# Optimization experiments

Hardware: AMD Instinct MI355X
Metric: run time of the kernel (lower is better)

The kernel has to match this reference:

```python
import jax, jax.numpy as jnp
import numpy as np

C, N, KS = 64, 64, 3  # channels, spatial size, kernel size (matches init_kwargs)
B = 4


def identity_kernel(c, k):
    # 'full' identity kernel: delta at spatial center on the channel diagonal
    ker = np.zeros((c, c, k, k), np.float32)
    ker[np.arange(c), np.arange(c), k // 2, k // 2] = 1.0
    return jnp.asarray(ker)


def setup_inputs() -> dict:
    key = jax.random.key(0)
    k1, k2, k3 = jax.random.split(key, 3)
    conv_in = jax.random.normal(k1, (B, C, N, N), jnp.float32)
    # small kernel perturbation, as produced by a hypernetwork at near-init ('I + net')
    K = jax.random.normal(k2, (B, C, C, KS, KS), jnp.float32) * 0.05
    bias = jax.random.normal(k3, (B, C, 1, 1), jnp.float32)
    return {"conv_in": conv_in, "K": K, "bias": bias}


def _circ_conv_one(x, ker):
    # x: [c, n, n], ker: [co, ci, kh, kw]; circular-padded cross-correlation (torch conv2d semantics)
    p = KS // 2
    xp = jnp.pad(x, ((0, 0), (p, p), (p, p)), mode="wrap")
    out = jax.lax.conv_general_dilated(
        xp[None], ker, window_strides=(1, 1), padding="VALID",
        dimension_numbers=("NCHW", "OIHW", "NCHW"))
    return out[0]  # [c, n, n]


def reference(conv_in, K, bias):
    # kernel_init == 'I + net': add identity kernel
    Kfull = K + identity_kernel(C, KS)[None]  # [B, c, c, k, k]

    # batch spatial circular conv2D with per-sample kernels
    conv_out = jax.vmap(_circ_conv_one)(conv_in, Kfull) + bias  # [B, c, n, n]

    # spectral log-determinant of the circular conv operator:
    # embed kernel into n x n grid, FFT2 over space, then per-frequency c x c logdet.
    # (per-frequency phase factors from kernel centering have unit modulus, so
    #  log|det| is independent of the spatial alignment convention)
    Kpad = jnp.zeros((K.shape[0], C, C, N, N), K.dtype).at[..., :KS, :KS].set(Kfull)
    Khat = jnp.fft.fft2(Kpad)                    # [B, c, c, n, n] complex
    Khat = jnp.moveaxis(Khat, (1, 2), (3, 4))    # [B, n, n, c, c]
    _, logabsdet = jnp.linalg.slogdet(Khat)      # [B, n, n]
    logdet = jnp.sum(logabsdet, axis=(1, 2))     # [B]

    return conv_out, logdet
```

## Files before the change

### kernel.cpp

```cpp
#include <hip/hip_runtime.h>
#include <hip/hip_fp16.h>
#include <math.h>

#define CCH 64
#define NSP 64
#define TAU 0.5f

__global__ __launch_bounds__(256) void conv_kernel(
    const float* __restrict__ x, const float* __restrict__ K,
    const float* __restrict__ bias, float* __restrict__ out) {
  int bid = blockIdx.x;
  int b = bid >> 6, co = bid & 63;
  __shared__ float w[CCH * 9];
  __shared__ float tile[64 * 65];
  int t = threadIdx.x;

  for (int i = t; i < CCH * 9; i += 256) {
    float v = K[(size_t)((b * 64 + co) * 64) * 9 + i];
    if (i == co * 9 + 4) v += 1.0f;
    w[i] = v;
  }

  int ty = t >> 2;
  int tx = t & 3;
  int x0 = tx << 4;
  float bval = bias[b * 64 + co];
  float acc[16];
#pragma unroll
  for (int i = 0; i < 16; ++i) acc[i] = bval;

  const float* xb = x + (size_t)(b * 64) * 4096;
  for (int ci = 0; ci < 64; ++ci) {
    __syncthreads();
    const float* xc = xb + (size_t)ci * 4096;
#pragma unroll
    for (int j = 0; j < 16; ++j) {
      int i = t + 256 * j;
      tile[(i >> 6) * 65 + (i & 63)] = xc[i];
    }
    __syncthreads();

    float w0 = w[ci * 9 + 0], w1 = w[ci * 9 + 1], w2 = w[ci * 9 + 2];
    float w3 = w[ci * 9 + 3], w4 = w[ci * 9 + 4], w5 = w[ci * 9 + 5];
    float w6 = w[ci * 9 + 6], w7 = w[ci * 9 + 7], w8 = w[ci * 9 + 8];

    int ym = ((ty - 1) & 63) * 65;
    int yc = ty * 65;
    int yp = ((ty + 1) & 63) * 65;
    float in0[18], in1[18], in2[18];
#pragma unroll
    for (int ix = 0; ix < 18; ++ix) {
      int xx = (x0 + ix - 1) & 63;
      in0[ix] = tile[ym + xx];
      in1[ix] = tile[yc + xx];
      in2[ix] = tile[yp + xx];
    }
#pragma unroll
    for (int px = 0; px < 16; ++px) {
      float a = acc[px];
      a = fmaf(w0, in0[px], a); a = fmaf(w1, in0[px + 1], a); a = fmaf(w2, in0[px + 2], a);
      a = fmaf(w3, in1[px], a); a = fmaf(w4, in1[px + 1], a); a = fmaf(w5, in1[px + 2], a);
      a = fmaf(w6, in2[px], a); a = fmaf(w7, in2[px + 1], a); a = fmaf(w8, in2[px + 2], a);
      acc[px] = a;
    }
  }

  float* op = out + (size_t)(b * 64 + co) * 4096 + ty * 64 + x0;
#pragma unroll
  for (int i = 0; i < 16; i += 4) {
    *(float4*)(op + i) = make_float4(acc[i], acc[i + 1], acc[i + 2], acc[i + 3]);
  }
}

__device__ __forceinline__ int h2i(__half2 h) { int i; __builtin_memcpy(&i, &h, 4); return i; }
__device__ __forceinline__ __half2 i2h(int i) { __half2 h; __builtin_memcpy(&h, &i, 4); return h; }

__global__ __launch_bounds__(64, 3) void logdet_kernel(
    const float* __restrict__ K, float* __restrict__ logdet) {
  int bid = blockIdx.x;
  int u, v;
  if (bid < 33) { u = 0; v = bid; }
  else if (bid < 2017) { int q = bid - 33; u = 1 + (q >> 6); v = q & 63; }
  else { u = 32; v = bid - 2017; }
  float weight = (((u & 31) == 0) && ((v & 31) == 0)) ? 1.0f : 2.0f;
  int b = blockIdx.y;

  int r = threadIdx.x;

  float Ar[3], Ai[3], Br[3], Bi[3];
  {
    const float k2pi = -6.283185307179586f / 64.0f;
    float su, cu, sv, cv;
    __sincosf(k2pi * (float)u, &su, &cu);
    __sincosf(k2pi * (float)v, &sv, &cv);
    Ar[0] = 1.0f; Ai[0] = 0.0f; Ar[1] = cu; Ai[1] = su;
    Ar[2] = cu * cu - su * su; Ai[2] = 2.0f * cu * su;
    Br[0] = 1.0f; Bi[0] = 0.0f; Br[1] = cv; Bi[1] = sv;
    Br[2] = cv * cv - sv * sv; Bi[2] = 2.0f * cv * sv;
  }
  float wr[9], wi[9];
#pragma unroll
  for (int kh = 0; kh < 3; ++kh)
#pragma unroll
    for (int kw = 0; kw < 3; ++kw) {
      wr[kh * 3 + kw] = Ar[kh] * Br[kw] - Ai[kh] * Bi[kw];
      wi[kh * 3 + kw] = Ar[kh] * Bi[kw] + Ai[kh] * Br[kw];
    }

  __half2 a2[65];
  const float4* Kp4 = (const float4*)(K + (size_t)(b * 64 + r) * 576);
#pragma unroll
  for (int g = 0; g < 16; ++g) {
    float f[36];
#pragma unroll
    for (int qq = 0; qq < 9; ++qq) {
      float4 vv = Kp4[g * 9 + qq];
      f[qq * 4 + 0] = vv.x; f[qq * 4 + 1] = vv.y; f[qq * 4 + 2] = vv.z; f[qq * 4 + 3] = vv.w;
    }
#pragma unroll
    for (int cc = 0; cc < 4; ++cc) {
      int c = g * 4 + cc;
      float re = 0.0f, im = 0.0f;
#pragma unroll
      for (int t9 = 0; t9 < 9; ++t9) {
        float kv = f[cc * 9 + t9];
        re = fmaf(kv, wr[t9], re);
        im = fmaf(kv, wi[t9], im);
      }
      if (c == r) { re += wr[4]; im += wi[4]; }
      a2[c] = __floats2half2_rn(re, im);
    }
  }
  a2[64] = __floats2half2_rn(0.0f, 0.0f);

  bool active = true;
  float pivmag = 1.0f;

  for (int k = 0; k < 63; ++k) {
    float fr0 = __low2float(a2[0]);
    float fi0 = __high2float(a2[0]);
    float mag = fmaf(fr0, fr0, fi0 * fi0);
    bool cand = active && (mag >= TAU);
    unsigned long long candm = __ballot(cand);
    int p;
    if (candm != 0ULL) {
      p = __ffsll(candm) - 1;
    } else {
      float mm = active ? mag : -1.0f;
#pragma unroll
      for (int off = 32; off > 0; off >>= 1) mm = fmaxf(mm, __shfl_xor(mm, off));
      unsigned long long mx = __ballot(active && (mag == mm));
      if (mx == 0ULL) mx = __ballot(active);
      p = __ffsll(mx) - 1;
    }
    p = __builtin_amdgcn_readfirstlane(p) & 63;

    bool isPiv = (r == p);
    pivmag = isPiv ? mag : pivmag;
    active = active && !isPiv;

    __half2 pivh = i2h(__builtin_amdgcn_readlane(h2i(a2[0]), p));
    float pr = __low2float(pivh);
    float pi = __high2float(pivh);
    float inv = __builtin_amdgcn_rcpf(fmaf(pr, pr, pi * pi));
    float fre = (fr0 * pr + fi0 * pi) * inv;
    float fim = (fi0 * pr - fr0 * pi) * inv;
    fre = active ? fre : 0.0f;
    fim = active ? fim : 0.0f;
    __half2 nfre2 = __float2half2_rn(-fre);
    __half2 fim2 = __halves2half2(__float2half_rn(fim),
                                  __float2half_rn(-fim));

    int rem = 63 - k;
#pragma unroll
    for (int ch = 0; ch < 8; ++ch) {
      if (ch * 8 < rem) {
        int c0 = ch * 8 + 1;
        int Li[8];
#pragma unroll
        for (int e = 0; e < 8; ++e)
          Li[e] = __builtin_amdgcn_readlane(h2i(a2[c0 + e]), p);
#pragma unroll
        for (int e = 0; e < 8; ++e) {
          __half2 P = i2h(Li[e]);
          __half2 tmp = __hfma2(nfre2, P, a2[c0 + e]);
          a2[c0 + e - 1] = __hfma2(fim2, __lowhigh2highlow(P), tmp);
        }
      }
    }
  }
  {
    float fr0 = __low2float(a2[0]);
    float fi0 = __high2float(a2[0]);
    if (active) pivmag = fmaf(fr0, fr0, fi0 * fi0);
  }

  float logsum = 0.5f * __logf(pivmag);
#pragma unroll
  for (int off = 32; off > 0; off >>= 1) logsum += __shfl_xor(logsum, off);
  if (r == 0) atomicAdd(&logdet[b], weight * logsum);
}

extern "C" void kernel_launch(void* const* d_in, const int* in_sizes, int n_in,
                              void* d_out, int out_size, void* d_ws, size_t ws_size,
                              hipStream_t stream) {
  const float* conv_in = (const float*)d_in[0];
  const float* K       = (const float*)d_in[1];
  const float* bias    = (const float*)d_in[2];
  float* out = (float*)d_out;
  float* logdet = out + 1048576;

  hipMemsetAsync(logdet, 0, 4 * sizeof(float), stream);
  conv_kernel<<<dim3(256), dim3(256), 0, stream>>>(conv_in, K, bias, out);
  logdet_kernel<<<dim3(2050, 4), dim3(64), 0, stream>>>(K, logdet);
}
```

Before: 371.7 us.

## Fuse conv and logdet into one launch with interleaved block roles

Merges the convolution kernel and the spectral logdet kernel into a single launch. Every ninth block performs a conv output channel and the rest perform logdet frequencies, so the two workloads run on the GPU at the same time. Each logdet block now handles all four batch samples for one frequency, one wavefront per sample, instead of one 64-thread block per (frequency, batch) pair. This removes a launch and the serialization between the two kernels. In exchange, the register budget is now shared between both roles under launch bounds of (256, 2), which could reduce occupancy or cause spills in the register-heavy logdet path.

```diff
diff --git a/kernel.cpp b/kernel.cpp
--- a/kernel.cpp
+++ b/kernel.cpp
@@ -2,90 +2,100 @@
 #include <hip/hip_fp16.h>
 #include <math.h>
 
-#define CCH 64
-#define NSP 64
 #define TAU 0.5f
-
-__global__ __launch_bounds__(256) void conv_kernel(
-    const float* __restrict__ x, const float* __restrict__ K,
-    const float* __restrict__ bias, float* __restrict__ out) {
-  int bid = blockIdx.x;
-  int b = bid >> 6, co = bid & 63;
-  __shared__ float w[CCH * 9];
-  __shared__ float tile[64 * 65];
-  int t = threadIdx.x;
-
-  for (int i = t; i < CCH * 9; i += 256) {
-    float v = K[(size_t)((b * 64 + co) * 64) * 9 + i];
-    if (i == co * 9 + 4) v += 1.0f;
-    w[i] = v;
-  }
-
-  int ty = t >> 2;
-  int tx = t & 3;
-  int x0 = tx << 4;
-  float bval = bias[b * 64 + co];
-  float acc[16];
-#pragma unroll
-  for (int i = 0; i < 16; ++i) acc[i] = bval;
-
-  const float* xb = x + (size_t)(b * 64) * 4096;
-  for (int ci = 0; ci < 64; ++ci) {
-    __syncthreads();
-    const float* xc = xb + (size_t)ci * 4096;
-#pragma unroll
-    for (int j = 0; j < 16; ++j) {
-      int i = t + 256 * j;
-      tile[(i >> 6) * 65 + (i & 63)] = xc[i];
-    }
-    __syncthreads();
-
-    float w0 = w[ci * 9 + 0], w1 = w[ci * 9 + 1], w2 = w[ci * 9 + 2];
-    float w3 = w[ci * 9 + 3], w4 = w[ci * 9 + 4], w5 = w[ci * 9 + 5];
-    float w6 = w[ci * 9 + 6], w7 = w[ci * 9 + 7], w8 = w[ci * 9 + 8];
-
-    int ym = ((ty - 1) & 63) * 65;
-    int yc = ty * 65;
-    int yp = ((ty + 1) & 63) * 65;
-    float in0[18], in1[18], in2[18];
-#pragma unroll
-    for (int ix = 0; ix < 18; ++ix) {
-      int xx = (x0 + ix - 1) & 63;
-      in0[ix] = tile[ym + xx];
-      in1[ix] = tile[yc + xx];
-      in2[ix] = tile[yp + xx];
-    }
-#pragma unroll
-    for (int px = 0; px < 16; ++px) {
-      float a = acc[px];
-      a = fmaf(w0, in0[px], a); a = fmaf(w1, in0[px + 1], a); a = fmaf(w2, in0[px + 2], a);
-      a = fmaf(w3, in1[px], a); a = fmaf(w4, in1[px + 1], a); a = fmaf(w5, in1[px + 2], a);
-      a = fmaf(w6, in2[px], a); a = fmaf(w7, in2[px + 1], a); a = fmaf(w8, in2[px + 2], a);
-      acc[px] = a;
-    }
-  }
-
-  float* op = out + (size_t)(b * 64 + co) * 4096 + ty * 64 + x0;
-#pragma unroll
-  for (int i = 0; i < 16; i += 4) {
-    *(float4*)(op + i) = make_float4(acc[i], acc[i + 1], acc[i + 2], acc[i + 3]);
-  }
-}
 
 __device__ __forceinline__ int h2i(__half2 h) { int i; __builtin_memcpy(&i, &h, 4); return i; }
 __device__ __forceinline__ __half2 i2h(int i) { __half2 h; __builtin_memcpy(&h, &i, 4); return h; }
 
-__global__ __launch_bounds__(64, 3) void logdet_kernel(
-    const float* __restrict__ K, float* __restrict__ logdet) {
+__global__ __launch_bounds__(256, 2) void fused_kernel(
+    const float* __restrict__ x, const float* __restrict__ K,
+    const float* __restrict__ bias, float* __restrict__ out,
+    float* __restrict__ logdet) {
+  __shared__ float smem[4736];
   int bid = blockIdx.x;
+  int t = threadIdx.x;
+
+  bool isConv = false;
+  int cid = 0, lid = 0;
+  if (bid < 2304) {
+    int q9 = bid / 9, m9 = bid - q9 * 9;
+    if (m9 == 8) { isConv = true; cid = q9; }
+    else lid = bid - (bid + 1) / 9;
+  } else {
+    lid = bid - 256;
+  }
+
+  if (isConv) {
+    int b = cid >> 6, co = cid & 63;
+    float* w = smem;
+    float* tile = smem + 576;
+
+    for (int i = t; i < 576; i += 256) {
+      float vv = K[(size_t)((b * 64 + co) * 64) * 9 + i];
+      if (i == co * 9 + 4) vv += 1.0f;
+      w[i] = vv;
+    }
+
+    int ty = t >> 2;
+    int tx = t & 3;
+    int x0 = tx << 4;
+    float bval = bias[b * 64 + co];
+    float acc[16];
+#pragma unroll
+    for (int i = 0; i < 16; ++i) acc[i] = bval;
+
+    const float* xb = x + (size_t)(b * 64) * 4096;
+    for (int ci = 0; ci < 64; ++ci) {
+      __syncthreads();
+      const float* xc = xb + (size_t)ci * 4096;
+#pragma unroll
+      for (int j = 0; j < 16; ++j) {
+        int i = t + 256 * j;
+        tile[(i >> 6) * 65 + (i & 63)] = xc[i];
+      }
+      __syncthreads();
+
+      float w0 = w[ci * 9 + 0], w1 = w[ci * 9 + 1], w2 = w[ci * 9 + 2];
+      float w3 = w[ci * 9 + 3], w4 = w[ci * 9 + 4], w5 = w[ci * 9 + 5];
+      float w6 = w[ci * 9 + 6], w7 = w[ci * 9 + 7], w8 = w[ci * 9 + 8];
+
+      int ym = ((ty - 1) & 63) * 65;
+      int yc = ty * 65;
+      int yp = ((ty + 1) & 63) * 65;
+      float in0[18], in1[18], in2[18];
+#pragma unroll
+      for (int ix = 0; ix < 18; ++ix) {
+        int xx = (x0 + ix - 1) & 63;
+        in0[ix] = tile[ym + xx];
+        in1[ix] = tile[yc + xx];
+        in2[ix] = tile[yp + xx];
+      }
+#pragma unroll
+      for (int px = 0; px < 16; ++px) {
+        float a = acc[px];
+        a = fmaf(w0, in0[px], a); a = fmaf(w1, in0[px + 1], a); a = fmaf(w2, in0[px + 2], a);
+        a = fmaf(w3, in1[px], a); a = fmaf(w4, in1[px + 1], a); a = fmaf(w5, in1[px + 2], a);
+        a = fmaf(w6, in2[px], a); a = fmaf(w7, in2[px + 1], a); a = fmaf(w8, in2[px + 2], a);
+        acc[px] = a;
+      }
+    }
+
+    float* op = out + (size_t)(b * 64 + co) * 4096 + ty * 64 + x0;
+#pragma unroll
+    for (int i = 0; i < 16; i += 4) {
+      *(float4*)(op + i) = make_float4(acc[i], acc[i + 1], acc[i + 2], acc[i + 3]);
+    }
+    return;
+  }
+
   int u, v;
-  if (bid < 33) { u = 0; v = bid; }
-  else if (bid < 2017) { int q = bid - 33; u = 1 + (q >> 6); v = q & 63; }
-  else { u = 32; v = bid - 2017; }
+  if (lid < 33) { u = 0; v = lid; }
+  else if (lid < 2017) { int q = lid - 33; u = 1 + (q >> 6); v = q & 63; }
+  else { u = 32; v = lid - 2017; }
   float weight = (((u & 31) == 0) && ((v & 31) == 0)) ? 1.0f : 2.0f;
-  int b = blockIdx.y;
-
-  int r = threadIdx.x;
+
+  int b = t >> 6;
+  int r = t & 63;
 
   float Ar[3], Ai[3], Br[3], Bi[3];
   {
@@ -211,6 +221,5 @@
   float* logdet = out + 1048576;
 
   hipMemsetAsync(logdet, 0, 4 * sizeof(float), stream);
-  conv_kernel<<<dim3(256), dim3(256), 0, stream>>>(conv_in, K, bias, out);
-  logdet_kernel<<<dim3(2050, 4), dim3(64), 0, stream>>>(K, logdet);
+  fused_kernel<<<dim3(2306), dim3(256), 0, stream>>>(conv_in, K, bias, out, logdet);
 }
```

After: 337.1 us. -9.3%, faster.
